# Performance work log

Hardware: AMD Instinct MI355X
Metric: run time of the kernel (lower is better)

Reference implementation:

```python
import jax, jax.numpy as jnp
import numpy as np

B, N = 4, 8192


def _nn_idx(a, b):
    # For each point in a [B,Na,3], index of nearest point in b [B,Nb,3].
    # ||a-b||^2 = ||a||^2 - 2 a.b + ||b||^2 ; ||a||^2 is constant per row -> drop it.
    d = jnp.sum(b * b, axis=-1)[:, None, :] - 2.0 * jnp.einsum('bnd,bmd->bnm', a, b)
    return jnp.argmin(d, axis=-1)  # [B, Na]


def _thickness(white, pial):
    # Mirrors compute_thickness_vector: white = inner, pial = outer.
    bix = jnp.arange(white.shape[0])[:, None]
    i1 = _nn_idx(white, pial)            # NN in pial for each white point
    inner_th = pial[bix, i1] - white     # [B, Nw, 3]
    i2 = _nn_idx(pial, white)            # NN in white for each pial point
    outer_th = pial - white[bix, i2]     # [B, Np, 3]
    return inner_th, outer_th


def _msn(a, b):
    # MeanSquaredNormLoss with w=None: mean over all points of sum((a-b)^2, -1)
    return jnp.mean(jnp.sum((a - b) ** 2, axis=-1))


def _sym(a, b, i_a, i_b):
    # SymmetricMeanSquaredNormLoss.forward (batch_size > 1 path, no weights)
    bix = jnp.arange(a.shape[0])[:, None]
    return 0.5 * (_msn(a, b[bix, i_a]) + _msn(a[bix, i_b], b))


def setup_inputs() -> dict:
    key = jax.random.key(0)
    ks = jax.random.split(key, 8)
    return {
        'pred_white': jax.random.normal(ks[0], (B, N, 3), jnp.float32),
        'pred_pial': jax.random.normal(ks[1], (B, N, 3), jnp.float32),
        'true_white': jax.random.normal(ks[2], (B, N, 3), jnp.float32),
        'true_pial': jax.random.normal(ks[3], (B, N, 3), jnp.float32),
        'i_pred_white': jax.random.randint(ks[4], (B, N), 0, N, jnp.int32),
        'i_true_white': jax.random.randint(ks[5], (B, N), 0, N, jnp.int32),
        'i_pred_pial': jax.random.randint(ks[6], (B, N), 0, N, jnp.int32),
        'i_true_pial': jax.random.randint(ks[7], (B, N), 0, N, jnp.int32),
    }


def reference(pred_white, pred_pial, true_white, true_pial,
              i_pred_white, i_true_white, i_pred_pial, i_true_pial):
    yp_inner, yp_outer = _thickness(pred_white, pred_pial)
    yt_inner, yt_outer = _thickness(true_white, true_pial)
    return (0.5 * _sym(yp_inner, yt_inner, i_pred_white, i_true_white)
            + 0.5 * _sym(yp_outer, yt_outer, i_pred_pial, i_true_pial))
```

## Files before the change

kernel.cpp:

```cpp
#include <hip/hip_runtime.h>
#include <math.h>

#define BATCH 4
#define NPTS 8192
#define BN (BATCH * NPTS)
#define NZB 16
#define QK 8
#define QBLK (256 * QK)
#define SUBT 64


__device__ __forceinline__ void pick_ab(int z, const float* pw, const float* pp,
                                        const float* tw, const float* tp,
                                        const float** qa, const float** cb) {
  if (z == 0)      { *qa = pw; *cb = pp; }
  else if (z == 1) { *qa = pp; *cb = pw; }
  else if (z == 2) { *qa = tw; *cb = tp; }
  else             { *qa = tp; *cb = tw; }
}

template <int SPL>
__global__ __launch_bounds__(256, 4) void nn_partial_kernel(
    const float* __restrict__ pw, const float* __restrict__ pp,
    const float* __restrict__ tw, const float* __restrict__ tp,
    float* __restrict__ part_d, unsigned char* __restrict__ part_t) {
  constexpr int SLICE = NPTS / SPL;
  constexpr int NSUB = SLICE / SUBT;
  __shared__ float4 sh[SLICE];

  const int zb = blockIdx.z;
  const int z = zb >> 2;
  const int b = zb & 3;
  const float* qa;
  const float* cb;
  pick_ab(z, pw, pp, tw, tp, &qa, &cb);

  const int tid = threadIdx.x;
  const int cslice = blockIdx.y * SLICE;
  const float* cbb = cb + (size_t)b * NPTS * 3;

  for (int m = tid; m < SLICE; m += 256) {
    const float* c = cbb + (size_t)(cslice + m) * 3;
    const float bx = c[0], by = c[1], bz = c[2];
    sh[m] = make_float4(bx, by, bz, fmaf(bx, bx, fmaf(by, by, bz * bz)));
  }
  __syncthreads();

  const int qbase = blockIdx.x * QBLK;
  float qx[QK], qy[QK], qz[QK], dmin[QK];
  int tile[QK];
  #pragma unroll
  for (int k = 0; k < QK; ++k) {
    const int n = qbase + tid + k * 256;
    const float* q = qa + ((size_t)b * NPTS + n) * 3;
    qx[k] = -2.0f * q[0];
    qy[k] = -2.0f * q[1];
    qz[k] = -2.0f * q[2];
    dmin[k] = INFINITY;
    tile[k] = 0;
  }

  for (int sub = 0; sub < NSUB; ++sub) {
    float pre[QK];
    #pragma unroll
    for (int k = 0; k < QK; ++k) pre[k] = dmin[k];

    const int cb0 = sub * SUBT;
    #pragma unroll 2
    for (int p = 0; p < SUBT / 2; ++p) {
      const float4 c0 = sh[cb0 + 2 * p];
      const float4 c1 = sh[cb0 + 2 * p + 1];
      float t0[QK], t1[QK];
      #pragma unroll
      for (int k = 0; k < QK; ++k)
        t0[k] = fmaf(qx[k], c0.x, fmaf(qy[k], c0.y, fmaf(qz[k], c0.z, c0.w)));
      #pragma unroll
      for (int k = 0; k < QK; ++k)
        t1[k] = fmaf(qx[k], c1.x, fmaf(qy[k], c1.y, fmaf(qz[k], c1.z, c1.w)));
      #pragma unroll
      for (int k = 0; k < QK; ++k)
        dmin[k] = fminf(fminf(t0[k], t1[k]), dmin[k]);
    }
    const int g = blockIdx.y * NSUB + sub;
    #pragma unroll
    for (int k = 0; k < QK; ++k)
      tile[k] = (dmin[k] < pre[k]) ? g : tile[k];
  }

  #pragma unroll
  for (int k = 0; k < QK; ++k) {
    const int n = qbase + tid + k * 256;
    const size_t o = (size_t)blockIdx.y * (NZB * NPTS) + (size_t)zb * NPTS + n;
    part_d[o] = dmin[k];
    part_t[o] = (unsigned char)tile[k];
  }
}

template <int SPL>
__global__ __launch_bounds__(256) void nn_merge_kernel(
    float* __restrict__ part_d, unsigned char* __restrict__ part_t,
    double* __restrict__ acc) {
  if (blockIdx.x == 0 && threadIdx.x == 0) *acc = 0.0;

  const int qid = blockIdx.x * 256 + threadIdx.x;
  float best_d = part_d[qid];
  int best_g = part_t[qid];
  #pragma unroll
  for (int s = 1; s < SPL; ++s) {
    const float d = part_d[(size_t)s * (NZB * NPTS) + qid];
    const int g = part_t[(size_t)s * (NZB * NPTS) + qid];
    if (d < best_d || (d == best_d && g < best_g)) { best_d = d; best_g = g; }
  }
  part_d[qid] = best_d;
  part_t[qid] = (unsigned char)best_g;
}

__global__ __launch_bounds__(1024) void nn_rescan_kernel(
    const float* __restrict__ pw, const float* __restrict__ pp,
    const float* __restrict__ tw, const float* __restrict__ tp,
    const float* __restrict__ part_d, const unsigned char* __restrict__ part_t,
    int* __restrict__ idx_all) {
  const int qid = (blockIdx.x * 1024 + threadIdx.x) >> 6;
  const int lane = threadIdx.x & 63;
  const int zb = qid >> 13;
  const int n = qid & (NPTS - 1);
  const int z = zb >> 2;
  const int b = zb & 3;
  const float* qa;
  const float* cb;
  pick_ab(z, pw, pp, tw, tp, &qa, &cb);

  const float best_d = part_d[qid];
  const int best_g = part_t[qid];

  const float* q = qa + ((size_t)b * NPTS + n) * 3;
  const float qx = -2.0f * q[0];
  const float qy = -2.0f * q[1];
  const float qz = -2.0f * q[2];
  const float* cbb = cb + (size_t)b * NPTS * 3;

  const int m = best_g * SUBT + lane;
  const float* c = cbb + (size_t)m * 3;
  const float bx = c[0], by = c[1], bz = c[2];
  const float b2 = fmaf(bx, bx, fmaf(by, by, bz * bz));
  const float dd = fmaf(qx, bx, fmaf(qy, by, fmaf(qz, bz, b2)));
  int idx = (dd == best_d) ? m : 0x7fffffff;
  #pragma unroll
  for (int off = 32; off > 0; off >>= 1)
    idx = min(idx, __shfl_down(idx, off));
  if (lane == 0) idx_all[qid] = idx;
}

__device__ __forceinline__ float3 ld3(const float* __restrict__ p, int i) {
  const float* q = p + (size_t)i * 3;
  return make_float3(q[0], q[1], q[2]);
}

__device__ __forceinline__ float diff_nrm2(float3 a1, float3 a2, float3 b1, float3 b2) {
  const float x = (a1.x - a2.x) - (b1.x - b2.x);
  const float y = (a1.y - a2.y) - (b1.y - b2.y);
  const float z = (a1.z - a2.z) - (b1.z - b2.z);
  return fmaf(x, x, fmaf(y, y, z * z));
}

__global__ __launch_bounds__(256) void loss_kernel(
    const float* __restrict__ pw, const float* __restrict__ pp,
    const float* __restrict__ tw, const float* __restrict__ tp,
    const int* __restrict__ ipw, const int* __restrict__ itw,
    const int* __restrict__ ipp, const int* __restrict__ itp,
    const int* __restrict__ idx_all, double* __restrict__ acc) {
  const int gid = blockIdx.x * 256 + threadIdx.x;
  const int term = blockIdx.y;
  const int b = gid >> 13;
  const int n = gid & (NPTS - 1);
  const int base = b * NPTS;

  const float* PW = pw + (size_t)base * 3;
  const float* PP = pp + (size_t)base * 3;
  const float* TW = tw + (size_t)base * 3;
  const float* TP = tp + (size_t)base * 3;
  const int* I1P = idx_all + (0 * BATCH + b) * NPTS;
  const int* I2P = idx_all + (1 * BATCH + b) * NPTS;
  const int* I1T = idx_all + (2 * BATCH + b) * NPTS;
  const int* I2T = idx_all + (3 * BATCH + b) * NPTS;

  float sv;
  if (term == 0) {
    const int j = ipw[base + n];
    sv = diff_nrm2(ld3(PP, I1P[n]), ld3(PW, n), ld3(TP, I1T[j]), ld3(TW, j));
  } else if (term == 1) {
    const int k = itw[base + n];
    sv = diff_nrm2(ld3(PP, I1P[k]), ld3(PW, k), ld3(TP, I1T[n]), ld3(TW, n));
  } else if (term == 2) {
    const int j = ipp[base + n];
    sv = diff_nrm2(ld3(PP, n), ld3(PW, I2P[n]), ld3(TP, j), ld3(TW, I2T[j]));
  } else {
    const int k = itp[base + n];
    sv = diff_nrm2(ld3(PP, k), ld3(PW, I2P[k]), ld3(TP, n), ld3(TW, I2T[n]));
  }

  double ds = (double)sv;
  #pragma unroll
  for (int o = 32; o > 0; o >>= 1) ds += __shfl_down(ds, o, 64);
  if ((threadIdx.x & 63) == 0) atomicAdd(acc, ds);
}

__global__ void finalize_kernel(const double* __restrict__ acc,
                                float* __restrict__ out) {
  out[0] = (float)(0.25 * (*acc) / (double)BN);
}

template <int SPL>
static void run_pipeline(const float* pw, const float* pp, const float* tw,
                         const float* tp, const int* ipw, const int* itw,
                         const int* ipp, const int* itp, char* ws, float* out,
                         hipStream_t stream) {
  double* acc = (double*)ws;
  int* idx_all = (int*)(ws + 64);
  float* part_d = (float*)(ws + 64 + (size_t)NZB * NPTS * 4);
  unsigned char* part_t =
      (unsigned char*)(ws + 64 + (size_t)NZB * NPTS * 4 +
                       (size_t)SPL * NZB * NPTS * 4);

  dim3 grid_nn(NPTS / QBLK, SPL, NZB);
  nn_partial_kernel<SPL><<<grid_nn, 256, 0, stream>>>(pw, pp, tw, tp, part_d,
                                                      part_t);
  nn_merge_kernel<SPL><<<(NZB * NPTS) / 256, 256, 0, stream>>>(part_d, part_t,
                                                               acc);
  nn_rescan_kernel<<<(NZB * NPTS) / 16, 1024, 0, stream>>>(
      pw, pp, tw, tp, part_d, part_t, idx_all);

  dim3 grid_loss(BN / 256, 4);
  loss_kernel<<<grid_loss, 256, 0, stream>>>(pw, pp, tw, tp, ipw, itw, ipp, itp,
                                             idx_all, acc);
  finalize_kernel<<<1, 1, 0, stream>>>(acc, out);
}

extern "C" void kernel_launch(void* const* d_in, const int* in_sizes, int n_in,
                              void* d_out, int out_size, void* d_ws, size_t ws_size,
                              hipStream_t stream) {
  const float* pw = (const float*)d_in[0];
  const float* pp = (const float*)d_in[1];
  const float* tw = (const float*)d_in[2];
  const float* tp = (const float*)d_in[3];
  const int* ipw = (const int*)d_in[4];
  const int* itw = (const int*)d_in[5];
  const int* ipp = (const int*)d_in[6];
  const int* itp = (const int*)d_in[7];
  char* ws = (char*)d_ws;
  float* out = (float*)d_out;

  const size_t base_need = 64 + (size_t)NZB * NPTS * 4;
  const size_t per_spl = (size_t)NZB * NPTS * 5;
  if (ws_size >= base_need + 32 * per_spl) {
    run_pipeline<32>(pw, pp, tw, tp, ipw, itw, ipp, itp, ws, out, stream);
  } else if (ws_size >= base_need + 16 * per_spl) {
    run_pipeline<16>(pw, pp, tw, tp, ipw, itw, ipp, itp, ws, out, stream);
  } else {
    run_pipeline<8>(pw, pp, tw, tp, ipw, itw, ipp, itp, ws, out, stream);
  }
}
```

Baseline: 206.5 us.

## Fuse merge with rescan and fold finalize into loss via ticket

Merges the per-split partial minima and rescans the winning 64-point tile in a single kernel. Each block stores the merged result in shared memory, and each wavefront then loops over 64 queries and uses a ballot to find the first matching index. The finalize kernel is removed: the last block of the loss kernel, found with an atomic ticket counter, writes the output. The goal is to drop two kernel launches and the global round trip of merged partials, at the cost of a serial per-wave loop over queries and extra atomics.

```diff
diff --git a/kernel.cpp b/kernel.cpp
--- a/kernel.cpp
+++ b/kernel.cpp
@@ -97,58 +97,64 @@
 }
 
 template <int SPL>
-__global__ __launch_bounds__(256) void nn_merge_kernel(
-    float* __restrict__ part_d, unsigned char* __restrict__ part_t,
-    double* __restrict__ acc) {
-  if (blockIdx.x == 0 && threadIdx.x == 0) *acc = 0.0;
-
-  const int qid = blockIdx.x * 256 + threadIdx.x;
-  float best_d = part_d[qid];
-  int best_g = part_t[qid];
-  #pragma unroll
-  for (int s = 1; s < SPL; ++s) {
-    const float d = part_d[(size_t)s * (NZB * NPTS) + qid];
-    const int g = part_t[(size_t)s * (NZB * NPTS) + qid];
-    if (d < best_d || (d == best_d && g < best_g)) { best_d = d; best_g = g; }
-  }
-  part_d[qid] = best_d;
-  part_t[qid] = (unsigned char)best_g;
-}
-
-__global__ __launch_bounds__(1024) void nn_rescan_kernel(
+__global__ __launch_bounds__(256) void nn_merge_rescan_kernel(
     const float* __restrict__ pw, const float* __restrict__ pp,
     const float* __restrict__ tw, const float* __restrict__ tp,
     const float* __restrict__ part_d, const unsigned char* __restrict__ part_t,
-    int* __restrict__ idx_all) {
-  const int qid = (blockIdx.x * 1024 + threadIdx.x) >> 6;
-  const int lane = threadIdx.x & 63;
-  const int zb = qid >> 13;
-  const int n = qid & (NPTS - 1);
+    int* __restrict__ idx_all, double* __restrict__ acc,
+    unsigned int* __restrict__ ticket) {
+  __shared__ float sd[256];
+  __shared__ int sg[256];
+
+  if (blockIdx.x == 0 && threadIdx.x == 0) { *acc = 0.0; *ticket = 0u; }
+
+  const int tid = threadIdx.x;
+  const int qbase = blockIdx.x * 256;
+  const int qid = qbase + tid;
+
+  {
+    float best_d = part_d[qid];
+    int best_g = part_t[qid];
+    #pragma unroll
+    for (int s = 1; s < SPL; ++s) {
+      const float d = part_d[(size_t)s * (NZB * NPTS) + qid];
+      const int g = part_t[(size_t)s * (NZB * NPTS) + qid];
+      if (d < best_d || (d == best_d && g < best_g)) { best_d = d; best_g = g; }
+    }
+    sd[tid] = best_d;
+    sg[tid] = best_g;
+  }
+  __syncthreads();
+
+  const int zb = qbase >> 13;
+  const int n0 = qbase & (NPTS - 1);
   const int z = zb >> 2;
   const int b = zb & 3;
   const float* qa;
   const float* cb;
   pick_ab(z, pw, pp, tw, tp, &qa, &cb);
-
-  const float best_d = part_d[qid];
-  const int best_g = part_t[qid];
-
-  const float* q = qa + ((size_t)b * NPTS + n) * 3;
-  const float qx = -2.0f * q[0];
-  const float qy = -2.0f * q[1];
-  const float qz = -2.0f * q[2];
+  const float* qb0 = qa + (size_t)b * NPTS * 3;
   const float* cbb = cb + (size_t)b * NPTS * 3;
 
-  const int m = best_g * SUBT + lane;
-  const float* c = cbb + (size_t)m * 3;
-  const float bx = c[0], by = c[1], bz = c[2];
-  const float b2 = fmaf(bx, bx, fmaf(by, by, bz * bz));
-  const float dd = fmaf(qx, bx, fmaf(qy, by, fmaf(qz, bz, b2)));
-  int idx = (dd == best_d) ? m : 0x7fffffff;
-  #pragma unroll
-  for (int off = 32; off > 0; off >>= 1)
-    idx = min(idx, __shfl_down(idx, off));
-  if (lane == 0) idx_all[qid] = idx;
+  const int w = tid >> 6;
+  const int lane = tid & 63;
+  for (int j = 0; j < 64; ++j) {
+    const int lq = w * 64 + j;
+    const float best_d = sd[lq];
+    const int best_g = sg[lq];
+    const float* q = qb0 + (size_t)(n0 + lq) * 3;
+    const float qx = -2.0f * q[0];
+    const float qy = -2.0f * q[1];
+    const float qz = -2.0f * q[2];
+    const int m = best_g * SUBT + lane;
+    const float* c = cbb + (size_t)m * 3;
+    const float bx = c[0], by = c[1], bz = c[2];
+    const float b2 = fmaf(bx, bx, fmaf(by, by, bz * bz));
+    const float dd = fmaf(qx, bx, fmaf(qy, by, fmaf(qz, bz, b2)));
+    const unsigned long long hit = __ballot(dd == best_d);
+    if (lane == 0)
+      idx_all[qbase + lq] = best_g * SUBT + (__ffsll((long long)hit) - 1);
+  }
 }
 
 __device__ __forceinline__ float3 ld3(const float* __restrict__ p, int i) {
@@ -163,12 +169,13 @@
   return fmaf(x, x, fmaf(y, y, z * z));
 }
 
-__global__ __launch_bounds__(256) void loss_kernel(
+__global__ __launch_bounds__(256) void loss_final_kernel(
     const float* __restrict__ pw, const float* __restrict__ pp,
     const float* __restrict__ tw, const float* __restrict__ tp,
     const int* __restrict__ ipw, const int* __restrict__ itw,
     const int* __restrict__ ipp, const int* __restrict__ itp,
-    const int* __restrict__ idx_all, double* __restrict__ acc) {
+    const int* __restrict__ idx_all, double* __restrict__ acc,
+    unsigned int* __restrict__ ticket, float* __restrict__ out) {
   const int gid = blockIdx.x * 256 + threadIdx.x;
   const int term = blockIdx.y;
   const int b = gid >> 13;
@@ -203,11 +210,17 @@
   #pragma unroll
   for (int o = 32; o > 0; o >>= 1) ds += __shfl_down(ds, o, 64);
   if ((threadIdx.x & 63) == 0) atomicAdd(acc, ds);
-}
-
-__global__ void finalize_kernel(const double* __restrict__ acc,
-                                float* __restrict__ out) {
-  out[0] = (float)(0.25 * (*acc) / (double)BN);
+
+  __threadfence();
+  __syncthreads();
+  if (threadIdx.x == 0) {
+    const unsigned int total = gridDim.x * gridDim.y;
+    const unsigned int old = atomicAdd(ticket, 1u);
+    if (old == total - 1u) {
+      const double t = atomicAdd(acc, 0.0);
+      out[0] = (float)(0.25 * t / (double)BN);
+    }
+  }
 }
 
 template <int SPL>
@@ -216,6 +229,7 @@
                          const int* ipp, const int* itp, char* ws, float* out,
                          hipStream_t stream) {
   double* acc = (double*)ws;
+  unsigned int* ticket = (unsigned int*)(ws + 8);
   int* idx_all = (int*)(ws + 64);
   float* part_d = (float*)(ws + 64 + (size_t)NZB * NPTS * 4);
   unsigned char* part_t =
@@ -225,15 +239,12 @@
   dim3 grid_nn(NPTS / QBLK, SPL, NZB);
   nn_partial_kernel<SPL><<<grid_nn, 256, 0, stream>>>(pw, pp, tw, tp, part_d,
                                                       part_t);
-  nn_merge_kernel<SPL><<<(NZB * NPTS) / 256, 256, 0, stream>>>(part_d, part_t,
-                                                               acc);
-  nn_rescan_kernel<<<(NZB * NPTS) / 16, 1024, 0, stream>>>(
-      pw, pp, tw, tp, part_d, part_t, idx_all);
+  nn_merge_rescan_kernel<SPL><<<(NZB * NPTS) / 256, 256, 0, stream>>>(
+      pw, pp, tw, tp, part_d, part_t, idx_all, acc, ticket);
 
   dim3 grid_loss(BN / 256, 4);
-  loss_kernel<<<grid_loss, 256, 0, stream>>>(pw, pp, tw, tp, ipw, itw, ipp, itp,
-                                             idx_all, acc);
-  finalize_kernel<<<1, 1, 0, stream>>>(acc, out);
+  loss_final_kernel<<<grid_loss, 256, 0, stream>>>(
+      pw, pp, tw, tp, ipw, itw, ipp, itp, idx_all, acc, ticket, out);
 }
 
 extern "C" void kernel_launch(void* const* d_in, const int* in_sizes, int n_in,
```

After: 222.3 us. +7.6%, slower.
